# Performance work log

Hardware: AMD Instinct MI355X
Metric: run time of the kernel (lower is better)

The kernel has to match this reference:

```python
import jax, jax.numpy as jnp
import numpy as np

N, E = 10000, 320000
IN_D, HID, OUT_D, EIN, KH = 128, 32, 128, 1, 32
BN_EPS = 1e-5  # torch BatchNorm1d default eps


def bn(x, g, b):
    # training-mode batch norm with biased variance (torch normalization semantics)
    m = jnp.mean(x, axis=0)
    v = jnp.mean((x - m) ** 2, axis=0)
    return g * (x - m) / jnp.sqrt(v + BN_EPS) + b


def setup_inputs() -> dict:
    key = jax.random.key(0)
    ks = jax.random.split(key, 8)

    def w(k, shape, s=0.05):
        return jax.random.normal(k, shape, dtype=jnp.float32) * s

    return {
        "H": jax.random.normal(ks[0], (N, IN_D), dtype=jnp.float32),
        "edge_attr": jax.random.normal(ks[1], (E, EIN), dtype=jnp.float32),
        "edges": jax.random.randint(ks[2], (2, E), 0, N),
        # linear1: input_dim -> hidden_dim
        "w1": w(ks[3], (HID, IN_D)), "b1": jnp.zeros((HID,), jnp.float32),
        # kernel MLP: edge_input_dim -> kernel_hidden -> (hidden+1)*hidden
        "kw1": w(ks[4], (KH, EIN)), "kb1": jnp.zeros((KH,), jnp.float32),
        "kw2": w(ks[5], ((HID + 1) * HID, KH)), "kb2": jnp.zeros(((HID + 1) * HID,), jnp.float32),
        # linear2: hidden -> output
        "w2": w(ks[6], (OUT_D, HID)), "b2": jnp.zeros((OUT_D,), jnp.float32),
        # batchnorm affine params
        "g_in": jnp.ones((IN_D,), jnp.float32), "beta_in": jnp.zeros((IN_D,), jnp.float32),
        "g_msg": jnp.ones((HID,), jnp.float32), "beta_msg": jnp.zeros((HID,), jnp.float32),
        "g_upd": jnp.ones((HID,), jnp.float32), "beta_upd": jnp.zeros((HID,), jnp.float32),
        "g_out": jnp.ones((OUT_D,), jnp.float32), "beta_out": jnp.zeros((OUT_D,), jnp.float32),
    }


def reference(H, edge_attr, edges, w1, b1, kw1, kb1, kw2, kb2, w2, b2,
              g_in, beta_in, g_msg, beta_msg, g_upd, beta_upd, g_out, beta_out):
    node_out, node_in = edges[0], edges[1]

    Hn = bn(H, g_in, beta_in)                    # input_batch_norm
    layer_input = jax.nn.relu(Hn)                # dropout -> identity (eval)

    # message: gather -> linear1 -> BN -> relu
    msg = layer_input[node_in] @ w1.T + b1       # [E, HID]
    msg = jax.nn.relu(bn(msg, g_msg, beta_msg))

    # edge-conditioned dynamic kernel: [E, HID+1, HID]
    kern = jax.nn.relu(edge_attr @ kw1.T + kb1) @ kw2.T + kb2
    kern = kern.reshape(E, HID + 1, HID)
    # per-edge matvec + per-edge bias row
    msg = jnp.einsum('ejk,ek->ej', kern[:, 1:, :], msg) + kern[:, 0, :]

    # aggregate: scatter_add into nodes
    upd = jax.ops.segment_sum(msg, node_out, num_segments=N)
    upd = jax.nn.relu(bn(upd, g_upd, beta_upd))

    out = upd @ w2.T + b2                        # linear2
    return bn(out, g_out, beta_out)              # output_batch_norm
```

## Files before the change

kernel.cpp:

```cpp
#include <hip/hip_runtime.h>
#include <math.h>

constexpr int N_    = 10000;
constexpr int E_    = 320000;
constexpr int IND   = 128;
constexpr int HID   = 32;
constexpr int OUTD  = 128;
constexpr int NIV   = 33;
constexpr float EPS = 1e-5f;

constexpr size_t OFF_SUMH   = 0;
constexpr size_t OFF_SQH    = 128;
constexpr size_t OFF_SUMP   = 256;
constexpr size_t OFF_SQP    = 288;
constexpr size_t OFF_SUMU   = 320;
constexpr size_t OFF_SQU    = 352;
constexpr size_t OFF_SUMO   = 384;
constexpr size_t OFF_SQO    = 512;
constexpr size_t OFF_OCC    = 640;
constexpr size_t OFF_DEGIN  = 704;
constexpr size_t OFF_DEGOUT = 10704;
constexpr size_t ZERO_CNT   = 20704;
constexpr size_t OFF_STARTS = 20740;
constexpr size_t OFF_CUR    = 30744;
constexpr size_t OFF_C1     = 40744;
constexpr size_t OFF_C0     = 75592;
constexpr size_t OFF_P      = 110440;
constexpr size_t OFF_UPD    = 430440;
constexpr size_t OFF_SORT   = 750440;
constexpr size_t OFF_IDX    = 1070440;

__device__ inline int compute_bps(const float* kw1, const float* kb1, float* bp) {
    int m = 0;
    for (int k = 0; k < 32; ++k) {
        float w = kw1[k];
        if (w != 0.f) bp[m++] = -kb1[k] / w;
    }
    for (int a = 1; a < m; ++a) {
        float v = bp[a]; int b = a - 1;
        while (b >= 0 && bp[b] > v) { bp[b+1] = bp[b]; --b; }
        bp[b+1] = v;
    }
    return m;
}

__global__ __launch_bounds__(256)
void k_A(const float* __restrict__ H,
         const float* __restrict__ ea, const int* __restrict__ edges,
         const float* __restrict__ kw1, const float* __restrict__ kb1,
         const float* __restrict__ kw2, const float* __restrict__ kb2,
         float* __restrict__ ws) {
    __shared__ float sel1[32], sel0[32];
    __shared__ float shS[256], shQ[256];
    __shared__ int locc[NIV];
    __shared__ float bps[32];
    __shared__ int sm;
    int* wsi = (int*)ws;
    int t = threadIdx.x;
    int bid = blockIdx.x;

    if (bid < 33) {
        int i = bid;
        if (t == 0) {
            float bp[32];
            int m = compute_bps(kw1, kb1, bp);
            float arep;
            if (m == 0 || i > m) arep = 0.f;
            else if (i == 0)     arep = bp[0]   - (1.f + 0.5f*fabsf(bp[0]));
            else if (i == m)     arep = bp[m-1] + (1.f + 0.5f*fabsf(bp[m-1]));
            else                 arep = (bp[i-1] < bp[i]) ? 0.5f*(bp[i-1] + bp[i]) : bp[i-1];
            for (int k = 0; k < 32; ++k) {
                bool s = (arep * kw1[k] + kb1[k]) > 0.f;
                sel1[k] = s ? kw1[k] : 0.f;
                sel0[k] = s ? kb1[k] : 0.f;
            }
        }
        __syncthreads();
        for (int r = t; r < 1056; r += 256) {
            float a1 = 0.f, a0 = 0.f;
            for (int k = 0; k < 32; ++k) {
                float w = kw2[r*32 + k];
                a1 += w * sel1[k];
                a0 += w * sel0[k];
            }
            ws[OFF_C1 + (size_t)i*1056 + r] = a1;
            ws[OFF_C0 + (size_t)i*1056 + r] = a0 + kb2[r];
        }
    } else if (bid < 161) {
        int b2 = bid - 33;
        int col = t & 127, half = t >> 7;
        float s = 0.f, q = 0.f;
        for (int r = b2*2 + half; r < N_; r += 128*2) {
            float x = H[(size_t)r*IND + col];
            s += x; q += x*x;
        }
        shS[t] = s; shQ[t] = q;
        __syncthreads();
        if (t < 128) {
            atomicAdd(&ws[OFF_SUMH + t], shS[t] + shS[t+128]);
            atomicAdd(&ws[OFF_SQH  + t], shQ[t] + shQ[t+128]);
        }
    } else {
        int b2 = bid - 161;
        if (t < NIV) locc[t] = 0;
        if (t == 0) {
            float bp[32];
            int m = compute_bps(kw1, kb1, bp);
            for (int k = 0; k < 32; ++k) bps[k] = (k < m) ? bp[k] : 0.f;
            sm = m;
        }
        __syncthreads();
        int m = sm;
        for (int e = b2*256 + t; e < E_; e += 313*256) {
            float a = ea[e];
            int cnt = 0;
            for (int k = 0; k < m; ++k) cnt += (bps[k] < a) ? 1 : 0;
            wsi[OFF_IDX + e] = cnt;
            atomicAdd(&locc[cnt], 1);
            atomicAdd(&wsi[OFF_DEGIN  + edges[E_ + e]], 1);
            atomicAdd(&wsi[OFF_DEGOUT + edges[e]],      1);
        }
        __syncthreads();
        if (t < NIV && locc[t] > 0) atomicAdd(&wsi[OFF_OCC + t], locc[t]);
    }
}

__global__ __launch_bounds__(256)
void k_B(const float* __restrict__ H, const float* __restrict__ w1,
         const float* __restrict__ b1, const float* __restrict__ g_in,
         const float* __restrict__ beta_in, float* __restrict__ ws) {
    __shared__ float w1L[32*129];
    __shared__ float xl[8][128];
    __shared__ int part[256];
    int* wsi = (int*)ws;
    int t = threadIdx.x;

    if (blockIdx.x == 0) {
        int base = t * 40;
        int loc[40];
        int s = 0;
        for (int i = 0; i < 40; ++i) {
            int idx = base + i;
            int v = (idx < N_) ? wsi[OFF_DEGOUT + idx] : 0;
            loc[i] = s; s += v;
        }
        part[t] = s;
        __syncthreads();
        for (int off = 1; off < 256; off <<= 1) {
            int add = (t >= off) ? part[t - off] : 0;
            __syncthreads();
            part[t] += add;
            __syncthreads();
        }
        int pre = (t > 0) ? part[t-1] : 0;
        for (int i = 0; i < 40; ++i) {
            int idx = base + i;
            if (idx <= N_) {
                int v = pre + loc[i];
                wsi[OFF_STARTS + idx] = v;
                if (idx < N_) wsi[OFF_CUR + idx] = v;
            }
        }
        return;
    }

    int g = t >> 5, j = t & 31;
    for (int idx = t; idx < 4096; idx += 256)
        w1L[(idx >> 7)*129 + (idx & 127)] = w1[idx];

    int n = (blockIdx.x - 1)*8 + g;
    float4 h4 = ((const float4*)(H + (size_t)n*IND))[j];
    float4 m4 = ((const float4*)(ws + OFF_SUMH))[j];
    float4 q4 = ((const float4*)(ws + OFF_SQH))[j];
    float4 gg = ((const float4*)g_in)[j];
    float4 bb = ((const float4*)beta_in)[j];
    float4 xv;
    {
        float* hp = (float*)&h4; float* mp = (float*)&m4; float* qp = (float*)&q4;
        float* gp = (float*)&gg; float* bp = (float*)&bb; float* xp = (float*)&xv;
        for (int i = 0; i < 4; ++i) {
            float mean = mp[i] * (1.f/N_);
            float var  = qp[i] * (1.f/N_) - mean*mean;
            float istd = 1.f / sqrtf(var + EPS);
            float gc = gp[i]*istd, bc = bp[i] - mean*gc;
            xp[i] = fmaxf(fmaf(gc, hp[i], bc), 0.f);
        }
    }
    ((float4*)&xl[g][0])[j] = xv;
    __syncthreads();
    float p = b1[j];
    const float* wr = &w1L[j*129];
    const float* xr = &xl[g][0];
    #pragma unroll 8
    for (int k = 0; k < 128; ++k) p = fmaf(wr[k], xr[k], p);
    ws[OFF_P + (size_t)n*HID + j] = p;
}

__global__ __launch_bounds__(256)
void k_C(const int* __restrict__ edges, float* __restrict__ ws) {
    __shared__ float shS[256], shQ[256];
    int* wsi = (int*)ws;
    int t = threadIdx.x;
    if (blockIdx.x < 313) {
        int b2 = blockIdx.x;
        for (int e = b2*256 + t; e < E_; e += 313*256) {
            int nout = edges[e];
            int pos = atomicAdd(&wsi[OFF_CUR + nout], 1);
            wsi[OFF_SORT + pos] = e;
        }
    } else {
        int b2 = blockIdx.x - 313;
        int j = t & 31, cp = t >> 5;
        float s = 0.f, q = 0.f;
        for (int n = b2*8 + cp; n < N_; n += 64*8) {
            float w = (float)wsi[OFF_DEGIN + n];
            float p = ws[OFF_P + (size_t)n*HID + j];
            s += w*p; q += w*p*p;
        }
        shS[t] = s; shQ[t] = q;
        __syncthreads();
        if (t < 32) {
            float S = 0.f, Qq = 0.f;
            for (int c = 0; c < 8; ++c) { S += shS[t + 32*c]; Qq += shQ[t + 32*c]; }
            atomicAdd(&ws[OFF_SUMP + t], S);
            atomicAdd(&ws[OFF_SQP  + t], Qq);
        }
    }
}

__global__ __launch_bounds__(256)
void k_D(const float* __restrict__ ea, const int* __restrict__ edges,
         const float* __restrict__ g_msg, const float* __restrict__ beta_msg,
         float* __restrict__ ws) {
    __shared__ float A[4][32*33];
    __shared__ float Bv[4][32];
    __shared__ float zl[8][4][32];
    __shared__ float shS[256], shQ[256];
    __shared__ int s_slot0, s_slot1;
    int* wsi = (int*)ws;
    int t = threadIdx.x, g = t >> 5, j = t & 31;

    if (t == 0) {
        int a0 = -1, a1 = -1;
        for (int i = 0; i < NIV; ++i)
            if (wsi[OFF_OCC + i] > 0) { if (a0 < 0) a0 = i; else if (a1 < 0) a1 = i; }
        s_slot0 = a0; s_slot1 = a1;
    }
    __syncthreads();
    int s0 = s_slot0, s1 = s_slot1;

    for (int idx = t; idx < 1024; idx += 256) {
        int jj = idx >> 5, kk = idx & 31;
        A[0][jj*33+kk] = (s0 >= 0) ? ws[OFF_C1 + (size_t)s0*1056 + 32 + idx] : 0.f;
        A[1][jj*33+kk] = (s0 >= 0) ? ws[OFF_C0 + (size_t)s0*1056 + 32 + idx] : 0.f;
        A[2][jj*33+kk] = (s1 >= 0) ? ws[OFF_C1 + (size_t)s1*1056 + 32 + idx] : 0.f;
        A[3][jj*33+kk] = (s1 >= 0) ? ws[OFF_C0 + (size_t)s1*1056 + 32 + idx] : 0.f;
    }
    if (t < 32) {
        Bv[0][t] = (s0 >= 0) ? ws[OFF_C1 + (size_t)s0*1056 + t] : 0.f;
        Bv[1][t] = (s0 >= 0) ? ws[OFF_C0 + (size_t)s0*1056 + t] : 0.f;
        Bv[2][t] = (s1 >= 0) ? ws[OFF_C1 + (size_t)s1*1056 + t] : 0.f;
        Bv[3][t] = (s1 >= 0) ? ws[OFF_C0 + (size_t)s1*1056 + t] : 0.f;
    }
    float mP = ws[OFF_SUMP + j] * (1.f/E_);
    float vP = ws[OFF_SQP  + j] * (1.f/E_) - mP*mP;
    float istd = 1.f / sqrtf(vP + EPS);
    float gc = g_msg[j]*istd, bc = beta_msg[j] - mP*gc;
    __syncthreads();

    int n = blockIdx.x*8 + g;
    int st = wsi[OFF_STARTS + n], en = wsi[OFF_STARTS + n + 1];
    float za0 = 0.f, zb0 = 0.f, za1 = 0.f, zb1 = 0.f;
    float suma0 = 0.f, suma1 = 0.f, rfall = 0.f;
    int c0 = 0, c1 = 0;
    for (int p = st; p < en; ++p) {
        int e   = wsi[OFF_SORT + p];
        float a = ea[e];
        int iv  = wsi[OFF_IDX + e];
        int nin = edges[E_ + e];
        float pv = ws[OFF_P + (size_t)nin*HID + j];
        float q  = fmaxf(fmaf(gc, pv, bc), 0.f);
        if (iv == s0)      { za0 = fmaf(a, q, za0); zb0 += q; suma0 += a; ++c0; }
        else if (iv == s1) { za1 = fmaf(a, q, za1); zb1 += q; suma1 += a; ++c1; }
        else {
            const float* C1r = ws + OFF_C1 + (size_t)iv*1056;
            const float* C0r = ws + OFF_C0 + (size_t)iv*1056;
            float d1 = 0.f, d0 = 0.f;
            for (int k = 0; k < 32; ++k) {
                float qk = __shfl(q, k, 32);
                d1 += C1r[32 + j*32 + k] * qk;
                d0 += C0r[32 + j*32 + k] * qk;
            }
            rfall += a*(d1 + C1r[j]) + (d0 + C0r[j]);
        }
    }
    zl[g][0][j] = za0; zl[g][1][j] = zb0; zl[g][2][j] = za1; zl[g][3][j] = zb1;
    __syncthreads();

    float acc = rfall;
    if (s0 >= 0) acc += suma0*Bv[0][j] + (float)c0*Bv[1][j];
    if (s1 >= 0) acc += suma1*Bv[2][j] + (float)c1*Bv[3][j];
    const float* z0 = zl[g][0]; const float* z1 = zl[g][1];
    const float* z2 = zl[g][2]; const float* z3 = zl[g][3];
    #pragma unroll 4
    for (int k = 0; k < 32; ++k) {
        acc += A[0][j*33+k]*z0[k] + A[1][j*33+k]*z1[k]
             + A[2][j*33+k]*z2[k] + A[3][j*33+k]*z3[k];
    }
    ws[OFF_UPD + (size_t)n*HID + j] = acc;

    shS[t] = acc; shQ[t] = acc*acc;
    __syncthreads();
    if (t < 32) {
        float S = 0.f, Qq = 0.f;
        for (int c = 0; c < 8; ++c) { S += shS[t + 32*c]; Qq += shQ[t + 32*c]; }
        atomicAdd(&ws[OFF_SUMU + t], S);
        atomicAdd(&ws[OFF_SQU  + t], Qq);
    }
}

__global__ __launch_bounds__(256)
void k_F(const float* __restrict__ w2, const float* __restrict__ b2,
         const float* __restrict__ g_upd, const float* __restrict__ beta_upd,
         float* __restrict__ ws, float* __restrict__ out) {
    __shared__ float U[2][HID];
    __shared__ float shS[256], shQ[256];
    int t = threadIdx.x, nh = t >> 7, o = t & 127;
    float gc = 0.f, bc = 0.f;
    if (o < 32) {
        float m = ws[OFF_SUMU + o]*(1.f/N_);
        float v = ws[OFF_SQU  + o]*(1.f/N_) - m*m;
        float istd = 1.f/sqrtf(v + EPS);
        gc = g_upd[o]*istd; bc = beta_upd[o] - m*gc;
    }
    float w2r[32];
    for (int k = 0; k < 32; ++k) w2r[k] = w2[o*32 + k];
    float bo = b2[o];
    float sO = 0.f, qO = 0.f;
    for (int base = blockIdx.x*2; base < N_; base += gridDim.x*2) {
        int n = base + nh;
        if (o < 32) {
            float u = ws[OFF_UPD + (size_t)n*HID + o];
            U[nh][o] = fmaxf(fmaf(gc, u, bc), 0.f);
        }
        __syncthreads();
        float v = bo;
        for (int k = 0; k < 32; ++k) v = fmaf(w2r[k], U[nh][k], v);
        out[(size_t)n*OUTD + o] = v;
        sO += v; qO += v*v;
        __syncthreads();
    }
    shS[t] = sO; shQ[t] = qO;
    __syncthreads();
    if (t < 128) {
        atomicAdd(&ws[OFF_SUMO + t], shS[t] + shS[t+128]);
        atomicAdd(&ws[OFF_SQO  + t], shQ[t] + shQ[t+128]);
    }
}

__global__ __launch_bounds__(256)
void k_G(const float* __restrict__ g_out, const float* __restrict__ beta_out,
         const float* __restrict__ ws, float* __restrict__ out) {
    int g = blockIdx.x*blockDim.x + threadIdx.x;
    if (g >= N_*OUTD) return;
    int o = g & 127;
    float m = ws[OFF_SUMO + o]*(1.f/N_);
    float v = ws[OFF_SQO  + o]*(1.f/N_) - m*m;
    float istd = 1.f/sqrtf(v + EPS);
    out[g] = g_out[o]*istd*(out[g] - m) + beta_out[o];
}

extern "C" void kernel_launch(void* const* d_in, const int* in_sizes, int n_in,
                              void* d_out, int out_size, void* d_ws, size_t ws_size,
                              hipStream_t stream) {
    const float* H        = (const float*)d_in[0];
    const float* ea       = (const float*)d_in[1];
    const int*   edges    = (const int*)  d_in[2];
    const float* w1       = (const float*)d_in[3];
    const float* b1       = (const float*)d_in[4];
    const float* kw1      = (const float*)d_in[5];
    const float* kb1      = (const float*)d_in[6];
    const float* kw2      = (const float*)d_in[7];
    const float* kb2      = (const float*)d_in[8];
    const float* w2       = (const float*)d_in[9];
    const float* b2       = (const float*)d_in[10];
    const float* g_in     = (const float*)d_in[11];
    const float* beta_in  = (const float*)d_in[12];
    const float* g_msg    = (const float*)d_in[13];
    const float* beta_msg = (const float*)d_in[14];
    const float* g_upd    = (const float*)d_in[15];
    const float* beta_upd = (const float*)d_in[16];
    const float* g_out    = (const float*)d_in[17];
    const float* beta_out = (const float*)d_in[18];
    float* ws  = (float*)d_ws;
    float* out = (float*)d_out;

    hipMemsetAsync(d_ws, 0, ZERO_CNT*sizeof(float), stream);
    hipLaunchKernelGGL(k_A, dim3(474),  dim3(256), 0, stream, H, ea, edges, kw1, kb1, kw2, kb2, ws);
    hipLaunchKernelGGL(k_B, dim3(1251), dim3(256), 0, stream, H, w1, b1, g_in, beta_in, ws);
    hipLaunchKernelGGL(k_C, dim3(377),  dim3(256), 0, stream, edges, ws);
    hipLaunchKernelGGL(k_D, dim3(1250), dim3(256), 0, stream, ea, edges, g_msg, beta_msg, ws);
    hipLaunchKernelGGL(k_F, dim3(250),  dim3(256), 0, stream, w2, b2, g_upd, beta_upd, ws, out);
    hipLaunchKernelGGL(k_G, dim3((N_*OUTD + 255)/256), dim3(256), 0, stream, g_out, beta_out, ws, out);
}
```

Measured before the change: 298.2 us.

## Pack per-edge attr, source node and interval into sorted records for aggregation

The counting-sort scatter now writes a packed float2 record (edge attribute plus source node index and interval id in bit fields), sorted by destination, instead of an edge id. The aggregation kernel no longer does the dependent chain of sort-index, edge_attr, interval and edges lookups. Each warp loads up to 32 records cooperatively, broadcasts them with shuffles, and issues four P-row gathers at a time to overlap memory latency. The interval index is recomputed in k_C instead of stored by k_A. The packing assumes node ids fit in 16 bits and interval ids in the upper bits, which holds for N=10000 but depends on that size.

```diff
diff --git a/kernel.cpp b/kernel.cpp
--- a/kernel.cpp
+++ b/kernel.cpp
@@ -27,8 +27,7 @@
 constexpr size_t OFF_C0     = 75592;
 constexpr size_t OFF_P      = 110440;
 constexpr size_t OFF_UPD    = 430440;
-constexpr size_t OFF_SORT   = 750440;
-constexpr size_t OFF_IDX    = 1070440;
+constexpr size_t OFF_AEN    = 750440;
 
 __device__ inline int compute_bps(const float* kw1, const float* kb1, float* bp) {
     int m = 0;
@@ -54,7 +53,6 @@
     __shared__ float shS[256], shQ[256];
     __shared__ int locc[NIV];
     __shared__ float bps[32];
-    __shared__ int sm;
     int* wsi = (int*)ws;
     int t = threadIdx.x;
     int bid = blockIdx.x;
@@ -106,16 +104,14 @@
         if (t == 0) {
             float bp[32];
             int m = compute_bps(kw1, kb1, bp);
-            for (int k = 0; k < 32; ++k) bps[k] = (k < m) ? bp[k] : 0.f;
-            sm = m;
-        }
-        __syncthreads();
-        int m = sm;
+            for (int k = 0; k < 32; ++k) bps[k] = (k < m) ? bp[k] : 3.0e38f;
+        }
+        __syncthreads();
         for (int e = b2*256 + t; e < E_; e += 313*256) {
             float a = ea[e];
             int cnt = 0;
-            for (int k = 0; k < m; ++k) cnt += (bps[k] < a) ? 1 : 0;
-            wsi[OFF_IDX + e] = cnt;
+            #pragma unroll
+            for (int k = 0; k < 32; ++k) cnt += (bps[k] < a) ? 1 : 0;
             atomicAdd(&locc[cnt], 1);
             atomicAdd(&wsi[OFF_DEGIN  + edges[E_ + e]], 1);
             atomicAdd(&wsi[OFF_DEGOUT + edges[e]],      1);
@@ -197,16 +193,32 @@
 }
 
 __global__ __launch_bounds__(256)
-void k_C(const int* __restrict__ edges, float* __restrict__ ws) {
+void k_C(const float* __restrict__ ea, const int* __restrict__ edges,
+         const float* __restrict__ kw1, const float* __restrict__ kb1,
+         float* __restrict__ ws) {
     __shared__ float shS[256], shQ[256];
+    __shared__ float bps[32];
     int* wsi = (int*)ws;
     int t = threadIdx.x;
     if (blockIdx.x < 313) {
+        if (t == 0) {
+            float bp[32];
+            int m = compute_bps(kw1, kb1, bp);
+            for (int k = 0; k < 32; ++k) bps[k] = (k < m) ? bp[k] : 3.0e38f;
+        }
+        __syncthreads();
+        float2* aen = (float2*)(ws + OFF_AEN);
         int b2 = blockIdx.x;
         for (int e = b2*256 + t; e < E_; e += 313*256) {
-            int nout = edges[e];
+            int   nout = edges[e];
+            int   nin  = edges[E_ + e];
+            float a    = ea[e];
+            int iv = 0;
+            #pragma unroll
+            for (int k = 0; k < 32; ++k) iv += (bps[k] < a) ? 1 : 0;
             int pos = atomicAdd(&wsi[OFF_CUR + nout], 1);
-            wsi[OFF_SORT + pos] = e;
+            float2 rec; rec.x = a; rec.y = __int_as_float(nin | (iv << 16));
+            aen[pos] = rec;
         }
     } else {
         int b2 = blockIdx.x - 313;
@@ -229,8 +241,7 @@
 }
 
 __global__ __launch_bounds__(256)
-void k_D(const float* __restrict__ ea, const int* __restrict__ edges,
-         const float* __restrict__ g_msg, const float* __restrict__ beta_msg,
+void k_D(const float* __restrict__ g_msg, const float* __restrict__ beta_msg,
          float* __restrict__ ws) {
     __shared__ float A[4][32*33];
     __shared__ float Bv[4][32];
@@ -271,35 +282,54 @@
     int n = blockIdx.x*8 + g;
     int st = wsi[OFF_STARTS + n], en = wsi[OFF_STARTS + n + 1];
     float za0 = 0.f, zb0 = 0.f, za1 = 0.f, zb1 = 0.f;
-    float suma0 = 0.f, suma1 = 0.f, rfall = 0.f;
-    int c0 = 0, c1 = 0;
-    for (int p = st; p < en; ++p) {
-        int e   = wsi[OFF_SORT + p];
-        float a = ea[e];
-        int iv  = wsi[OFF_IDX + e];
-        int nin = edges[E_ + e];
-        float pv = ws[OFF_P + (size_t)nin*HID + j];
-        float q  = fmaxf(fmaf(gc, pv, bc), 0.f);
-        if (iv == s0)      { za0 = fmaf(a, q, za0); zb0 += q; suma0 += a; ++c0; }
-        else if (iv == s1) { za1 = fmaf(a, q, za1); zb1 += q; suma1 += a; ++c1; }
-        else {
-            const float* C1r = ws + OFF_C1 + (size_t)iv*1056;
-            const float* C0r = ws + OFF_C0 + (size_t)iv*1056;
-            float d1 = 0.f, d0 = 0.f;
-            for (int k = 0; k < 32; ++k) {
-                float qk = __shfl(q, k, 32);
-                d1 += C1r[32 + j*32 + k] * qk;
-                d0 += C0r[32 + j*32 + k] * qk;
+    float suma0 = 0.f, suma1 = 0.f, c0f = 0.f, c1f = 0.f, rfall = 0.f;
+    const float2* aen = (const float2*)(ws + OFF_AEN);
+
+    for (int base = st; base < en; base += 32) {
+        int cnt = en - base; if (cnt > 32) cnt = 32;
+        float a_j = 0.f; int meta_j = 0;
+        if (j < cnt) {
+            float2 r = aen[base + j];
+            a_j = r.x; meta_j = __float_as_int(r.y);
+        }
+        for (int k = 0; k < cnt; k += 4) {
+            float pv[4], aa[4]; int ivv[4]; bool val[4];
+            #pragma unroll
+            for (int u = 0; u < 4; ++u) {
+                int kk = (k + u) & 31;
+                aa[u]  = __shfl(a_j, kk, 32);
+                int mt = __shfl(meta_j, kk, 32);
+                val[u] = (k + u) < cnt;
+                int nin = mt & 0xFFFF; ivv[u] = mt >> 16;
+                pv[u] = ws[OFF_P + (size_t)nin*HID + j];
             }
-            rfall += a*(d1 + C1r[j]) + (d0 + C0r[j]);
+            #pragma unroll
+            for (int u = 0; u < 4; ++u) {
+                if (!val[u]) continue;
+                float q = fmaxf(fmaf(gc, pv[u], bc), 0.f);
+                float a = aa[u]; int iv = ivv[u];
+                if (iv == s0)      { za0 = fmaf(a, q, za0); zb0 += q; suma0 += a; c0f += 1.f; }
+                else if (iv == s1) { za1 = fmaf(a, q, za1); zb1 += q; suma1 += a; c1f += 1.f; }
+                else {
+                    const float* C1r = ws + OFF_C1 + (size_t)iv*1056;
+                    const float* C0r = ws + OFF_C0 + (size_t)iv*1056;
+                    float d1 = 0.f, d0 = 0.f;
+                    for (int k2 = 0; k2 < 32; ++k2) {
+                        float qk = __shfl(q, k2, 32);
+                        d1 += C1r[32 + j*32 + k2] * qk;
+                        d0 += C0r[32 + j*32 + k2] * qk;
+                    }
+                    rfall += a*(d1 + C1r[j]) + (d0 + C0r[j]);
+                }
+            }
         }
     }
     zl[g][0][j] = za0; zl[g][1][j] = zb0; zl[g][2][j] = za1; zl[g][3][j] = zb1;
     __syncthreads();
 
     float acc = rfall;
-    if (s0 >= 0) acc += suma0*Bv[0][j] + (float)c0*Bv[1][j];
-    if (s1 >= 0) acc += suma1*Bv[2][j] + (float)c1*Bv[3][j];
+    if (s0 >= 0) acc += suma0*Bv[0][j] + c0f*Bv[1][j];
+    if (s1 >= 0) acc += suma1*Bv[2][j] + c1f*Bv[3][j];
     const float* z0 = zl[g][0]; const float* z1 = zl[g][1];
     const float* z2 = zl[g][2]; const float* z3 = zl[g][3];
     #pragma unroll 4
@@ -398,8 +428,8 @@
     hipMemsetAsync(d_ws, 0, ZERO_CNT*sizeof(float), stream);
     hipLaunchKernelGGL(k_A, dim3(474),  dim3(256), 0, stream, H, ea, edges, kw1, kb1, kw2, kb2, ws);
     hipLaunchKernelGGL(k_B, dim3(1251), dim3(256), 0, stream, H, w1, b1, g_in, beta_in, ws);
-    hipLaunchKernelGGL(k_C, dim3(377),  dim3(256), 0, stream, edges, ws);
-    hipLaunchKernelGGL(k_D, dim3(1250), dim3(256), 0, stream, ea, edges, g_msg, beta_msg, ws);
+    hipLaunchKernelGGL(k_C, dim3(377),  dim3(256), 0, stream, ea, edges, kw1, kb1, ws);
+    hipLaunchKernelGGL(k_D, dim3(1250), dim3(256), 0, stream, g_msg, beta_msg, ws);
     hipLaunchKernelGGL(k_F, dim3(250),  dim3(256), 0, stream, w2, b2, g_upd, beta_upd, ws, out);
     hipLaunchKernelGGL(k_G, dim3((N_*OUTD + 255)/256), dim3(256), 0, stream, g_out, beta_out, ws, out);
 }
```

Measured after the change: 257.9 us. -13.5%, faster.
